# Performance work log

Measured on AMD Instinct MI355X. Metric: run time of the kernel, lower is better.

Reference implementation:

```python
import jax, jax.numpy as jnp
import numpy as np

D_MODEL = 256
NHEAD = 4
HEAD_DIM = D_MODEL // NHEAD
TEMP = float(np.sqrt(D_MODEL / NHEAD))
EPS = 1e-5


def layernorm(x, g, b):
    mu = jnp.mean(x, axis=-1, keepdims=True)
    var = jnp.mean(jnp.square(x - mu), axis=-1, keepdims=True)
    return (x - mu) * jax.lax.rsqrt(var + EPS) * g + b


def setup_inputs() -> dict:
    key = jax.random.key(0)
    ks = jax.random.split(key, 8)
    B, S, D = 4, 4096, D_MODEL
    s = 1.0 / np.sqrt(D)
    return {
        "x": jax.random.normal(ks[0], (B, S, D), dtype=jnp.float32),
        "Wq": jax.random.normal(ks[1], (D, D), dtype=jnp.float32) * s,
        "Wk": jax.random.normal(ks[2], (D, D), dtype=jnp.float32) * s,
        "Wv": jax.random.normal(ks[3], (D, D), dtype=jnp.float32) * s,
        "g1": jnp.ones((D,), jnp.float32),
        "b1": jnp.zeros((D,), jnp.float32),
        "g2": jnp.ones((D,), jnp.float32),
        "b2": jnp.zeros((D,), jnp.float32),
        "W1": jax.random.normal(ks[4], (D, D), dtype=jnp.float32) * s,
        "bf1": jnp.zeros((D,), jnp.float32),
        "W2": jax.random.normal(ks[5], (D, D), dtype=jnp.float32) * s,
        "bf2": jnp.zeros((D,), jnp.float32),
    }


def reference(x, Wq, Wk, Wv, g1, b1, g2, b2, W1, bf1, W2, bf2):
    B, S, D = x.shape
    xn = layernorm(x, g1, b1)
    # torch Linear (no bias): y = x @ W.T
    q = (xn @ Wq.T).reshape(B, S, NHEAD, HEAD_DIM)
    k = (xn @ Wk.T).reshape(B, S, NHEAD, HEAD_DIM)
    v = (xn @ Wv.T).reshape(B, S, NHEAD, HEAD_DIM)
    scores = jnp.einsum("bqhd,bkhd->bhqk", q, k) / TEMP
    causal = jnp.tril(jnp.ones((S, S), dtype=bool))  # True = keep
    scores = jnp.where(causal, scores, -jnp.inf)
    attn = jax.nn.softmax(scores, axis=-1)
    att = jnp.einsum("bhqk,bkhd->bqhd", attn, v).reshape(B, S, D)
    xt = x + att
    h = layernorm(xt, g2, b2)
    ffn = jax.nn.relu(h @ W1.T + bf1) @ W2.T + bf2
    return xt + ffn
```

## Files before the change

### kernel.cpp

```cpp
#include <hip/hip_runtime.h>
#include <math.h>

#define D_MODEL 256
#define NHEAD 4
#define HEAD_DIM 64
#define SEQ 4096
#define BATCH 4
#define MROWS (BATCH * SEQ)

typedef __attribute__((ext_vector_type(8))) short short8;
typedef __attribute__((ext_vector_type(4))) short short4v;
typedef __attribute__((ext_vector_type(8))) __bf16 bf16x8;
typedef __attribute__((ext_vector_type(4))) float f32x4;

__device__ inline short f2bf(float f) {
  unsigned u = __float_as_uint(f);
  u += 0x7fffu + ((u >> 16) & 1u);
  return (short)(u >> 16);
}
__device__ inline bf16x8 as_bf8(short8 s) {
  union { short8 s; bf16x8 b; } u;
  u.s = s;
  return u.b;
}
__device__ __forceinline__ void g2lds16(const void* g, void* l) {
  __builtin_amdgcn_global_load_lds(
      (const __attribute__((address_space(1))) unsigned int*)g,
      (__attribute__((address_space(3))) unsigned int*)l, 16, 0, 0);
}

__device__ __forceinline__ f32x4 mfma16bf(short4v a, short4v b, f32x4 c) {
#if __has_builtin(__builtin_amdgcn_mfma_f32_16x16x16bf16_1k)
  return __builtin_amdgcn_mfma_f32_16x16x16bf16_1k(a, b, c, 0, 0, 0);
#else
  asm("v_mfma_f32_16x16x16_bf16 %0, %1, %2, %0" : "+v"(c) : "v"(a), "v"(b));
  return c;
#endif
}

#define QSCALE 0.1803368801111204f

__global__ __launch_bounds__(256) void wcvt(const float* __restrict__ s0, const float* __restrict__ s1,
                                            const float* __restrict__ s2, const float* __restrict__ s3,
                                            const float* __restrict__ s4, short* __restrict__ d0,
                                            short* __restrict__ d1, short* __restrict__ d2,
                                            short* __restrict__ d3, short* __restrict__ d4) {
  int mat = blockIdx.x >> 5;
  int e = ((blockIdx.x & 31) * 256 + threadIdx.x) * 8;
  const float* s = mat == 0 ? s0 : mat == 1 ? s1 : mat == 2 ? s2 : mat == 3 ? s3 : s4;
  short* d = mat == 0 ? d0 : mat == 1 ? d1 : mat == 2 ? d2 : mat == 3 ? d3 : d4;
  int n = e >> 8, k0 = e & 255;
  float4 f0 = *(const float4*)(s + n * 256 + k0);
  float4 f1 = *(const float4*)(s + n * 256 + k0 + 4);
  short8 o = {f2bf(f0.x), f2bf(f0.y), f2bf(f0.z), f2bf(f0.w),
              f2bf(f1.x), f2bf(f1.y), f2bf(f1.z), f2bf(f1.w)};
  int chunk = k0 >> 5, g = (k0 >> 3) & 3;
  *(short8*)(d + n * 256 + chunk * 32 + ((g ^ (n & 3)) * 8)) = o;
}

__global__ __launch_bounds__(256) void ln_sw(const float* __restrict__ x,
                                             const float* __restrict__ g,
                                             const float* __restrict__ b,
                                             short* __restrict__ o) {
  int r = threadIdx.x >> 5, c8 = threadIdx.x & 31;
  int row = blockIdx.x * 8 + r;
  const float* xr = x + (size_t)row * D_MODEL + c8 * 8;
  float4 a = *(const float4*)xr;
  float4 c = *(const float4*)(xr + 4);
  float s = a.x + a.y + a.z + a.w + c.x + c.y + c.z + c.w;
#pragma unroll
  for (int off = 16; off > 0; off >>= 1) s += __shfl_xor(s, off);
  float mu = s * (1.0f / D_MODEL);
  float d0 = a.x - mu, d1 = a.y - mu, d2 = a.z - mu, d3 = a.w - mu;
  float d4 = c.x - mu, d5 = c.y - mu, d6 = c.z - mu, d7 = c.w - mu;
  float ss = d0 * d0 + d1 * d1 + d2 * d2 + d3 * d3 + d4 * d4 + d5 * d5 + d6 * d6 + d7 * d7;
#pragma unroll
  for (int off = 16; off > 0; off >>= 1) ss += __shfl_xor(ss, off);
  float rstd = rsqrtf(ss * (1.0f / D_MODEL) + 1e-5f);
  float4 ga = *(const float4*)(g + c8 * 8);
  float4 gc = *(const float4*)(g + c8 * 8 + 4);
  float4 ba = *(const float4*)(b + c8 * 8);
  float4 bc = *(const float4*)(b + c8 * 8 + 4);
  short8 ov = {f2bf(d0 * rstd * ga.x + ba.x), f2bf(d1 * rstd * ga.y + ba.y),
               f2bf(d2 * rstd * ga.z + ba.z), f2bf(d3 * rstd * ga.w + ba.w),
               f2bf(d4 * rstd * gc.x + bc.x), f2bf(d5 * rstd * gc.y + bc.y),
               f2bf(d6 * rstd * gc.z + bc.z), f2bf(d7 * rstd * gc.w + bc.w)};
  int chunk = c8 >> 2, gr = c8 & 3;
  *(short8*)(o + (size_t)row * D_MODEL + chunk * 32 + ((gr ^ (row & 3)) * 8)) = ov;
}

__global__ __launch_bounds__(256) void qkv_direct(
    const short* __restrict__ Wqi, const short* __restrict__ Wki,
    const short* __restrict__ Wvi, const short* __restrict__ Xn,
    short* __restrict__ qo, short* __restrict__ kimg, short* __restrict__ vimg) {
  __shared__ __align__(16) short Xs[64 * 256];
  const int t = threadIdx.x, lane = t & 63, w = t >> 6;
  const int l15 = lane & 15, quad = lane >> 4;
  const int m0 = blockIdx.x * 64;
  const int which = blockIdx.y;
  const short* Wb = which == 0 ? Wqi : which == 1 ? Wki : Wvi;

#pragma unroll
  for (int j = 0; j < 8; j++) {
    int so = __builtin_amdgcn_readfirstlane((w * 8 + j) * 512);
    g2lds16(Xn + (size_t)m0 * D_MODEL + so + lane * 8, &Xs[so]);
  }
  __syncthreads();

  const short* xb = &Xs[l15 * 256 + ((quad ^ (l15 & 3)) * 8)];
  const short* wb = Wb + (size_t)(w * 64 + l15) * 256 + ((quad ^ (l15 & 3)) * 8);

  f32x4 acc[4][4];
#pragma unroll
  for (int i = 0; i < 4; i++)
#pragma unroll
    for (int j = 0; j < 4; j++) acc[i][j] = (f32x4){0.f, 0.f, 0.f, 0.f};

#pragma unroll
  for (int kf = 0; kf < 8; kf++) {
    bf16x8 fx[4], fw[4];
#pragma unroll
    for (int i = 0; i < 4; i++) {
      fx[i] = as_bf8(*(const short8*)(xb + i * 4096 + kf * 32));
      fw[i] = as_bf8(*(const short8*)(wb + i * 4096 + kf * 32));
    }
    if (which == 2) {
#pragma unroll
      for (int mt = 0; mt < 4; mt++)
#pragma unroll
        for (int nt = 0; nt < 4; nt++)
          acc[mt][nt] = __builtin_amdgcn_mfma_f32_16x16x32_bf16(fx[mt], fw[nt], acc[mt][nt], 0, 0, 0);
    } else {
#pragma unroll
      for (int mt = 0; mt < 4; mt++)
#pragma unroll
        for (int nt = 0; nt < 4; nt++)
          acc[mt][nt] = __builtin_amdgcn_mfma_f32_16x16x32_bf16(fw[nt], fx[mt], acc[mt][nt], 0, 0, 0);
    }
  }

#pragma unroll
  for (int mt = 0; mt < 4; mt++)
#pragma unroll
    for (int nt = 0; nt < 4; nt++) {
      f32x4 v = acc[mt][nt];
      if (which == 2) {
        int n = w * 64 + nt * 16 + l15;
        int mr = m0 + mt * 16 + quad * 4;
        int b = mr >> 12, s = mr & 4095, h = n >> 6, d = n & 63;
        size_t off = ((size_t)(b * NHEAD + h) * 64 + (s >> 6)) * 4096 +
                     (size_t)d * 64 + ((((s & 63) >> 3) ^ (d & 7)) * 8) + (s & 7);
        short4v o = {f2bf(v[0]), f2bf(v[1]), f2bf(v[2]), f2bf(v[3])};
        *(short4v*)(vimg + off) = o;
      } else {
        int m = m0 + mt * 16 + l15;
        int nb = w * 64 + nt * 16 + quad * 4;
        if (which == 0) {
          v *= QSCALE;
          short4v o = {f2bf(v[0]), f2bf(v[1]), f2bf(v[2]), f2bf(v[3])};
          *(short4v*)(qo + (size_t)m * D_MODEL + nb) = o;
        } else {
          int b = m >> 12, s = m & 4095, h = nb >> 6, d = nb & 63;
          size_t off = ((size_t)(b * NHEAD + h) * 64 + (s >> 6)) * 4096 +
                       (size_t)(s & 63) * 64 + (((d >> 3) ^ (s & 7)) * 8) + (d & 7);
          short4v o = {f2bf(v[0]), f2bf(v[1]), f2bf(v[2]), f2bf(v[3])};
          *(short4v*)(kimg + off) = o;
        }
      }
    }
}

__global__ __launch_bounds__(256) void ffn_direct(
    const short* __restrict__ w1i, const short* __restrict__ w2i,
    const short* __restrict__ Hsw, const float* __restrict__ bf1,
    const float* __restrict__ bf2, const float* __restrict__ xt,
    float* __restrict__ out) {
  __shared__ __align__(16) short Hs[32 * 256];
  __shared__ __align__(16) short F1s[32 * 264];
  const int t = threadIdx.x, lane = t & 63, w = t >> 6;
  const int l15 = lane & 15, quad = lane >> 4;
  const int m0 = blockIdx.x * 32;

#pragma unroll
  for (int j = 0; j < 4; j++) {
    int so = __builtin_amdgcn_readfirstlane((w * 4 + j) * 512);
    g2lds16(Hsw + (size_t)m0 * D_MODEL + so + lane * 8, &Hs[so]);
  }
  __syncthreads();

  const short* hb = &Hs[l15 * 256 + ((quad ^ (l15 & 3)) * 8)];
  const short* w1b = w1i + (size_t)(w * 64 + l15) * 256 + ((quad ^ (l15 & 3)) * 8);
  const short* w2b = w2i + (size_t)(w * 64 + l15) * 256 + ((quad ^ (l15 & 3)) * 8);

  f32x4 a1[2][4];
#pragma unroll
  for (int i = 0; i < 2; i++)
#pragma unroll
    for (int j = 0; j < 4; j++) a1[i][j] = (f32x4){0.f, 0.f, 0.f, 0.f};
#pragma unroll
  for (int kf = 0; kf < 8; kf++) {
    bf16x8 fh[2], fw1[4];
#pragma unroll
    for (int i = 0; i < 2; i++) fh[i] = as_bf8(*(const short8*)(hb + i * 4096 + kf * 32));
#pragma unroll
    for (int i = 0; i < 4; i++) fw1[i] = as_bf8(*(const short8*)(w1b + i * 4096 + kf * 32));
#pragma unroll
    for (int mt = 0; mt < 2; mt++)
#pragma unroll
      for (int nt = 0; nt < 4; nt++)
        a1[mt][nt] = __builtin_amdgcn_mfma_f32_16x16x32_bf16(fw1[nt], fh[mt], a1[mt][nt], 0, 0, 0);
  }
#pragma unroll
  for (int mt = 0; mt < 2; mt++)
#pragma unroll
    for (int nt = 0; nt < 4; nt++) {
      int n1 = w * 64 + nt * 16 + quad * 4;
      int ml = mt * 16 + l15;
      float4 bv = *(const float4*)(bf1 + n1);
      f32x4 v = a1[mt][nt];
      short4v o = {f2bf(fmaxf(v[0] + bv.x, 0.f)), f2bf(fmaxf(v[1] + bv.y, 0.f)),
                   f2bf(fmaxf(v[2] + bv.z, 0.f)), f2bf(fmaxf(v[3] + bv.w, 0.f))};
      *(short4v*)&F1s[ml * 264 + n1] = o;
    }
  __syncthreads();

  const short* fb = &F1s[l15 * 264 + quad * 8];
  f32x4 a2[2][4];
#pragma unroll
  for (int i = 0; i < 2; i++)
#pragma unroll
    for (int j = 0; j < 4; j++) a2[i][j] = (f32x4){0.f, 0.f, 0.f, 0.f};
#pragma unroll
  for (int kf = 0; kf < 8; kf++) {
    bf16x8 ff[2], fw2[4];
#pragma unroll
    for (int i = 0; i < 2; i++) ff[i] = as_bf8(*(const short8*)(fb + i * 16 * 264 + kf * 32));
#pragma unroll
    for (int i = 0; i < 4; i++) fw2[i] = as_bf8(*(const short8*)(w2b + i * 4096 + kf * 32));
#pragma unroll
    for (int mt = 0; mt < 2; mt++)
#pragma unroll
      for (int nt = 0; nt < 4; nt++)
        a2[mt][nt] = __builtin_amdgcn_mfma_f32_16x16x32_bf16(ff[mt], fw2[nt], a2[mt][nt], 0, 0, 0);
  }
#pragma unroll
  for (int mt = 0; mt < 2; mt++)
#pragma unroll
    for (int nt = 0; nt < 4; nt++) {
      int n2 = w * 64 + nt * 16 + l15;
      int mg = m0 + mt * 16 + quad * 4;
      float bv = bf2[n2];
      f32x4 v = a2[mt][nt];
#pragma unroll
      for (int r = 0; r < 4; r++) {
        size_t a = (size_t)(mg + r) * D_MODEL + n2;
        out[a] = v[r] + bv + xt[a];
      }
    }
}

__global__ __launch_bounds__(256, 3) void attn_v7(const short* __restrict__ qb,
                                                  const short* __restrict__ kimg,
                                                  const short* __restrict__ vimg,
                                                  const float* __restrict__ x,
                                                  float* __restrict__ xt) {
  __shared__ __align__(16) short Ks[2 * 4096];
  __shared__ __align__(16) short Vs[2 * 4096];

  const int t = threadIdx.x, lane = t & 63, w = t >> 6;
  const int quad = lane >> 4, l15 = lane & 15, l7 = lane & 7;
  const int qa = quad & 1, q1 = quad >> 1;
  const int yy = blockIdx.y, gq = yy >> 4, rq = yy & 15;
  const int qt = gq == 0 ? 63 - rq : gq == 1 ? rq : gq == 2 ? 47 - rq : 16 + rq;
  const int bh = blockIdx.x, b = bh >> 2, h = bh & 3;
  const int ldsoff = __builtin_amdgcn_readfirstlane(w * 512);
  const short* kb_bh = kimg + (size_t)bh * 64 * 4096;
  const short* vb_bh = vimg + (size_t)bh * 64 * 4096;

  const int sb = w * 32;
  const int q0 = qt * 64;

  const short* ka[2][2];
#pragma unroll
  for (int kk = 0; kk < 2; kk++)
#pragma unroll
    for (int dh = 0; dh < 2; dh++)
      ka[kk][dh] = &Ks[(sb + kk * 16 + l15) * 64 + (((quad + 4 * dh) ^ l7) * 8)];
  const short* va[2];
#pragma unroll
  for (int kk = 0; kk < 2; kk++) {
    int sk = sb + kk * 16;
    va[kk] = &Vs[(sk >> 6) * 4096 + l15 * 64 + ((((((sk & 63) >> 3) | q1) ^ l7)) * 8) + qa * 4];
  }

  bf16x8 qf[4][2];
  {
    const short* qpb = qb + ((size_t)(b * SEQ + q0 + l15)) * D_MODEL + h * HEAD_DIM + quad * 8;
#pragma unroll
    for (int qq = 0; qq < 4; qq++) {
      qf[qq][0] = as_bf8(*(const short8*)(qpb + qq * 16 * D_MODEL));
      qf[qq][1] = as_bf8(*(const short8*)(qpb + qq * 16 * D_MODEL + 32));
    }
  }

  f32x4 oacc[4][4];
#pragma unroll
  for (int i = 0; i < 4; i++)
#pragma unroll
    for (int j = 0; j < 4; j++) oacc[i][j] = (f32x4){0.f, 0.f, 0.f, 0.f};
  float lrun[4] = {0.f, 0.f, 0.f, 0.f};

  const int niter = (qt + 2) >> 1;

#pragma unroll
  for (int i = 0; i < 4; i++) {
    g2lds16(kb_bh + i * 2048 + t * 8, &Ks[i * 2048 + ldsoff]);
    g2lds16(vb_bh + i * 2048 + t * 8, &Vs[i * 2048 + ldsoff]);
  }
  __syncthreads();

  for (int it = 0; it < niter; it++) {
    const int j0 = it * 128;
    const bool active = (j0 + sb) <= (q0 + 63);

    uint2 pu[2][4];
    if (active) {
      f32x4 st[2][4];
#pragma unroll
      for (int kk = 0; kk < 2; kk++) {
        bf16x8 k0 = as_bf8(*(const short8*)(ka[kk][0]));
        bf16x8 k1 = as_bf8(*(const short8*)(ka[kk][1]));
#pragma unroll
        for (int qq = 0; qq < 4; qq++) {
          f32x4 z = (f32x4){0.f, 0.f, 0.f, 0.f};
          z = __builtin_amdgcn_mfma_f32_16x16x32_bf16(k0, qf[qq][0], z, 0, 0, 0);
          z = __builtin_amdgcn_mfma_f32_16x16x32_bf16(k1, qf[qq][1], z, 0, 0, 0);
          st[kk][qq] = z;
        }
      }
      if (j0 + sb + 31 > q0) {
#pragma unroll
        for (int kk = 0; kk < 2; kk++) {
          int kbase = j0 + sb + kk * 16 + quad * 4;
#pragma unroll
          for (int qq = 0; qq < 4; qq++) {
            int qrow = q0 + qq * 16 + l15;
#pragma unroll
            for (int r = 0; r < 4; r++)
              if (kbase + r > qrow) st[kk][qq][r] = -1e30f;
          }
        }
      }
#pragma unroll
      for (int kk = 0; kk < 2; kk++)
#pragma unroll
        for (int qq = 0; qq < 4; qq++) {
          float p0 = __builtin_amdgcn_exp2f(st[kk][qq][0]);
          float p1 = __builtin_amdgcn_exp2f(st[kk][qq][1]);
          float p2 = __builtin_amdgcn_exp2f(st[kk][qq][2]);
          float p3 = __builtin_amdgcn_exp2f(st[kk][qq][3]);
          lrun[qq] += p0 + p1 + p2 + p3;
          pu[kk][qq].x = (__float_as_uint(p0) >> 16) | (__float_as_uint(p1) & 0xffff0000u);
          pu[kk][qq].y = (__float_as_uint(p2) >> 16) | (__float_as_uint(p3) & 0xffff0000u);
        }
    }

    __syncthreads();

    if (it + 1 < niter) {
      const short* kc_base = kb_bh + (size_t)(2 * (it + 1)) * 4096;
#pragma unroll
      for (int i = 0; i < 4; i++)
        g2lds16(kc_base + i * 2048 + t * 8, &Ks[i * 2048 + ldsoff]);
    }

    if (active) {
#pragma unroll
      for (int kk = 0; kk < 2; kk++) {
        union { uint2 u; short4v s; } pb0, pb1, pb2, pb3;
        pb0.u = pu[kk][0];
        pb1.u = pu[kk][1];
        pb2.u = pu[kk][2];
        pb3.u = pu[kk][3];
#pragma unroll
        for (int dt = 0; dt < 4; dt++) {
          short4v vv = *(const short4v*)(va[kk] + dt * 1024);
          oacc[dt][0] = mfma16bf(vv, pb0.s, oacc[dt][0]);
          oacc[dt][1] = mfma16bf(vv, pb1.s, oacc[dt][1]);
          oacc[dt][2] = mfma16bf(vv, pb2.s, oacc[dt][2]);
          oacc[dt][3] = mfma16bf(vv, pb3.s, oacc[dt][3]);
        }
      }
    }

    __syncthreads();

    if (it + 1 < niter) {
      const short* vc_base = vb_bh + (size_t)(2 * (it + 1)) * 4096;
#pragma unroll
      for (int i = 0; i < 4; i++)
        g2lds16(vc_base + i * 2048 + t * 8, &Vs[i * 2048 + ldsoff]);
    }
  }

#pragma unroll
  for (int qq = 0; qq < 4; qq++) {
    lrun[qq] += __shfl_xor(lrun[qq], 16);
    lrun[qq] += __shfl_xor(lrun[qq], 32);
  }
  float* ored = (float*)Ks;
  float* lred = (float*)Vs;
  __syncthreads();
  if (quad == 0) {
#pragma unroll
    for (int qq = 0; qq < 4; qq++) lred[(w * 4 + qq) * 16 + l15] = lrun[qq];
  }
#pragma unroll
  for (int rr = 1; rr < 4; rr++) {
#pragma unroll
    for (int dt = 0; dt < 4; dt++)
      if (dt == ((w + rr) & 3)) {
#pragma unroll
        for (int qq = 0; qq < 4; qq++)
#pragma unroll
          for (int e = 0; e < 4; e++)
            ored[dt * 1024 + (quad * 4 + e) * 64 + qq * 16 + l15] = oacc[dt][qq][e];
      }
    __syncthreads();
#pragma unroll
    for (int dt = 0; dt < 4; dt++)
      if (dt == w) {
#pragma unroll
        for (int qq = 0; qq < 4; qq++)
#pragma unroll
          for (int e = 0; e < 4; e++)
            oacc[dt][qq][e] += ored[dt * 1024 + (quad * 4 + e) * 64 + qq * 16 + l15];
      }
    if (rr < 3) __syncthreads();
  }
  float inv[4];
#pragma unroll
  for (int qq = 0; qq < 4; qq++) {
    float s = lred[qq * 16 + l15] + lred[(4 + qq) * 16 + l15] +
              lred[(8 + qq) * 16 + l15] + lred[(12 + qq) * 16 + l15];
    inv[qq] = 1.0f / s;
  }
#pragma unroll
  for (int dt = 0; dt < 4; dt++)
    if (dt == w) {
      size_t rowb = ((size_t)(b * SEQ + q0 + l15)) * D_MODEL + h * HEAD_DIM + dt * 16 + quad * 4;
#pragma unroll
      for (int qq = 0; qq < 4; qq++) {
        size_t a = rowb + (size_t)qq * 16 * D_MODEL;
        float4 xv = *(const float4*)(x + a);
        float4 o = make_float4(oacc[dt][qq][0] * inv[qq] + xv.x,
                               oacc[dt][qq][1] * inv[qq] + xv.y,
                               oacc[dt][qq][2] * inv[qq] + xv.z,
                               oacc[dt][qq][3] * inv[qq] + xv.w);
        *(float4*)(xt + a) = o;
      }
    }
}

extern "C" void kernel_launch(void* const* d_in, const int* in_sizes, int n_in,
                              void* d_out, int out_size, void* d_ws,
                              size_t ws_size, hipStream_t stream) {
  const float* x = (const float*)d_in[0];
  const float* Wq = (const float*)d_in[1];
  const float* Wk = (const float*)d_in[2];
  const float* Wv = (const float*)d_in[3];
  const float* g1 = (const float*)d_in[4];
  const float* b1 = (const float*)d_in[5];
  const float* g2 = (const float*)d_in[6];
  const float* b2 = (const float*)d_in[7];
  const float* W1 = (const float*)d_in[8];
  const float* bf1 = (const float*)d_in[9];
  const float* W2 = (const float*)d_in[10];
  const float* bf2 = (const float*)d_in[11];
  float* out = (float*)d_out;

  char* ws = (char*)d_ws;
  float* xt = (float*)ws;
  short* q_bf = (short*)(ws + (16u << 20));
  short* kimg = (short*)(ws + (24u << 20));
  short* vimg = (short*)(ws + (32u << 20));
  short* xn_sw = (short*)(ws + (40u << 20));
  short* wq_i = (short*)(ws + (48u << 20));
  short* wk_i = wq_i + 65536;
  short* wv_i = wq_i + 2 * 65536;
  short* w1_i = wq_i + 3 * 65536;
  short* w2_i = wq_i + 4 * 65536;

  dim3 blk(256);
  wcvt<<<160, blk, 0, stream>>>(Wq, Wk, Wv, W1, W2, wq_i, wk_i, wv_i, w1_i, w2_i);
  ln_sw<<<MROWS / 8, blk, 0, stream>>>(x, g1, b1, xn_sw);
  qkv_direct<<<dim3(MROWS / 64, 3), blk, 0, stream>>>(wq_i, wk_i, wv_i, xn_sw,
                                                      q_bf, kimg, vimg);
  attn_v7<<<dim3(16, 64), blk, 0, stream>>>(q_bf, kimg, vimg, x, xt);
  ln_sw<<<MROWS / 8, blk, 0, stream>>>(xt, g2, b2, xn_sw);
  ffn_direct<<<MROWS / 32, blk, 0, stream>>>(w1_i, w2_i, xn_sw, bf1, bf2, xt, out);
}
```

Baseline: 184.8 us.

## Register-prefetch K/V in attention and fuse second LayerNorm into FFN

The attention kernel no longer stages K/V tiles through shared memory with block-wide barriers. Each wave now loads its own K and V fragments straight from global memory into registers, double-buffered, so the next tile is fetched while the current one is being computed. This removes the per-iteration __syncthreads but raises register pressure, so launch bounds drop to 2 blocks per SM. Separately, the second LayerNorm is computed inside the FFN kernel, which removes one launch and the bf16 round trip of the normalized activations through global memory.

```diff
diff --git a/kernel.cpp b/kernel.cpp
--- a/kernel.cpp
+++ b/kernel.cpp
@@ -170,21 +170,46 @@
     }
 }
 
-__global__ __launch_bounds__(256) void ffn_direct(
+__global__ __launch_bounds__(256) void ffn_ln(
     const short* __restrict__ w1i, const short* __restrict__ w2i,
-    const short* __restrict__ Hsw, const float* __restrict__ bf1,
-    const float* __restrict__ bf2, const float* __restrict__ xt,
-    float* __restrict__ out) {
+    const float* __restrict__ g2v, const float* __restrict__ b2v,
+    const float* __restrict__ bf1, const float* __restrict__ bf2,
+    const float* __restrict__ xt, float* __restrict__ out) {
   __shared__ __align__(16) short Hs[32 * 256];
   __shared__ __align__(16) short F1s[32 * 264];
   const int t = threadIdx.x, lane = t & 63, w = t >> 6;
   const int l15 = lane & 15, quad = lane >> 4;
   const int m0 = blockIdx.x * 32;
 
-#pragma unroll
-  for (int j = 0; j < 4; j++) {
-    int so = __builtin_amdgcn_readfirstlane((w * 4 + j) * 512);
-    g2lds16(Hsw + (size_t)m0 * D_MODEL + so + lane * 8, &Hs[so]);
+  {
+    const int r = t >> 5, c8 = t & 31;
+    float4 ga = *(const float4*)(g2v + c8 * 8);
+    float4 gc = *(const float4*)(g2v + c8 * 8 + 4);
+    float4 ba = *(const float4*)(b2v + c8 * 8);
+    float4 bc = *(const float4*)(b2v + c8 * 8 + 4);
+#pragma unroll
+    for (int pass = 0; pass < 4; pass++) {
+      int row = pass * 8 + r;
+      const float* xr = xt + (size_t)(m0 + row) * D_MODEL + c8 * 8;
+      float4 a = *(const float4*)xr;
+      float4 c = *(const float4*)(xr + 4);
+      float s = a.x + a.y + a.z + a.w + c.x + c.y + c.z + c.w;
+#pragma unroll
+      for (int off = 16; off > 0; off >>= 1) s += __shfl_xor(s, off);
+      float mu = s * (1.0f / D_MODEL);
+      float d0 = a.x - mu, d1 = a.y - mu, d2 = a.z - mu, d3 = a.w - mu;
+      float d4 = c.x - mu, d5 = c.y - mu, d6 = c.z - mu, d7 = c.w - mu;
+      float ss = d0 * d0 + d1 * d1 + d2 * d2 + d3 * d3 + d4 * d4 + d5 * d5 + d6 * d6 + d7 * d7;
+#pragma unroll
+      for (int off = 16; off > 0; off >>= 1) ss += __shfl_xor(ss, off);
+      float rstd = rsqrtf(ss * (1.0f / D_MODEL) + 1e-5f);
+      short8 ov = {f2bf(d0 * rstd * ga.x + ba.x), f2bf(d1 * rstd * ga.y + ba.y),
+                   f2bf(d2 * rstd * ga.z + ba.z), f2bf(d3 * rstd * ga.w + ba.w),
+                   f2bf(d4 * rstd * gc.x + bc.x), f2bf(d5 * rstd * gc.y + bc.y),
+                   f2bf(d6 * rstd * gc.z + bc.z), f2bf(d7 * rstd * gc.w + bc.w)};
+      int chunk = c8 >> 2, gr = c8 & 3;
+      *(short8*)&Hs[row * 256 + chunk * 32 + ((gr ^ (row & 3)) * 8)] = ov;
+    }
   }
   __syncthreads();
 
@@ -259,13 +284,13 @@
     }
 }
 
-__global__ __launch_bounds__(256, 3) void attn_v7(const short* __restrict__ qb,
+__global__ __launch_bounds__(256, 2) void attn_v8(const short* __restrict__ qb,
                                                   const short* __restrict__ kimg,
                                                   const short* __restrict__ vimg,
                                                   const float* __restrict__ x,
                                                   float* __restrict__ xt) {
-  __shared__ __align__(16) short Ks[2 * 4096];
-  __shared__ __align__(16) short Vs[2 * 4096];
+  __shared__ __align__(16) float ored[4 * 1024];
+  __shared__ float lred[256];
 
   const int t = threadIdx.x, lane = t & 63, w = t >> 6;
   const int quad = lane >> 4, l15 = lane & 15, l7 = lane & 7;
@@ -273,24 +298,23 @@
   const int yy = blockIdx.y, gq = yy >> 4, rq = yy & 15;
   const int qt = gq == 0 ? 63 - rq : gq == 1 ? rq : gq == 2 ? 47 - rq : 16 + rq;
   const int bh = blockIdx.x, b = bh >> 2, h = bh & 3;
-  const int ldsoff = __builtin_amdgcn_readfirstlane(w * 512);
   const short* kb_bh = kimg + (size_t)bh * 64 * 4096;
   const short* vb_bh = vimg + (size_t)bh * 64 * 4096;
 
   const int sb = w * 32;
   const int q0 = qt * 64;
 
-  const short* ka[2][2];
+  int koff[2][2];
 #pragma unroll
   for (int kk = 0; kk < 2; kk++)
 #pragma unroll
     for (int dh = 0; dh < 2; dh++)
-      ka[kk][dh] = &Ks[(sb + kk * 16 + l15) * 64 + (((quad + 4 * dh) ^ l7) * 8)];
-  const short* va[2];
+      koff[kk][dh] = (sb + kk * 16 + l15) * 64 + (((quad + 4 * dh) ^ l7) * 8);
+  int voff[2];
 #pragma unroll
   for (int kk = 0; kk < 2; kk++) {
     int sk = sb + kk * 16;
-    va[kk] = &Vs[(sk >> 6) * 4096 + l15 * 64 + ((((((sk & 63) >> 3) | q1) ^ l7)) * 8) + qa * 4];
+    voff[kk] = (sk >> 6) * 4096 + l15 * 64 + ((((sk & 63) >> 3) | q1) ^ l7) * 8 + qa * 4;
   }
 
   bf16x8 qf[4][2];
@@ -312,24 +336,31 @@
 
   const int niter = (qt + 2) >> 1;
 
-#pragma unroll
-  for (int i = 0; i < 4; i++) {
-    g2lds16(kb_bh + i * 2048 + t * 8, &Ks[i * 2048 + ldsoff]);
-    g2lds16(vb_bh + i * 2048 + t * 8, &Vs[i * 2048 + ldsoff]);
-  }
-  __syncthreads();
-
-  for (int it = 0; it < niter; it++) {
+  bf16x8 kA[2][2], kB[2][2];
+  short4v vA[2][4], vB[2][4];
+
+  if (sb <= q0 + 63) {
+#pragma unroll
+    for (int kk = 0; kk < 2; kk++) {
+#pragma unroll
+      for (int dh = 0; dh < 2; dh++)
+        kA[kk][dh] = as_bf8(*(const short8*)(kb_bh + koff[kk][dh]));
+#pragma unroll
+      for (int dt = 0; dt < 4; dt++)
+        vA[kk][dt] = *(const short4v*)(vb_bh + voff[kk] + dt * 1024);
+    }
+  }
+
+  auto body = [&](bf16x8(&KC)[2][2], short4v(&VC)[2][4], bf16x8(&KN)[2][2],
+                  short4v(&VN)[2][4], int it) {
     const int j0 = it * 128;
     const bool active = (j0 + sb) <= (q0 + 63);
-
-    uint2 pu[2][4];
+    const bool pnext = (it + 1 < niter) && ((j0 + 128 + sb) <= (q0 + 63));
+    f32x4 st[2][4];
     if (active) {
-      f32x4 st[2][4];
 #pragma unroll
       for (int kk = 0; kk < 2; kk++) {
-        bf16x8 k0 = as_bf8(*(const short8*)(ka[kk][0]));
-        bf16x8 k1 = as_bf8(*(const short8*)(ka[kk][1]));
+        bf16x8 k0 = KC[kk][0], k1 = KC[kk][1];
 #pragma unroll
         for (int qq = 0; qq < 4; qq++) {
           f32x4 z = (f32x4){0.f, 0.f, 0.f, 0.f};
@@ -338,6 +369,21 @@
           st[kk][qq] = z;
         }
       }
+    }
+    if (pnext) {
+      const short* kbp = kb_bh + (size_t)(it + 1) * 8192;
+      const short* vbp = vb_bh + (size_t)(it + 1) * 8192;
+#pragma unroll
+      for (int kk = 0; kk < 2; kk++) {
+#pragma unroll
+        for (int dh = 0; dh < 2; dh++)
+          KN[kk][dh] = as_bf8(*(const short8*)(kbp + koff[kk][dh]));
+#pragma unroll
+        for (int dt = 0; dt < 4; dt++)
+          VN[kk][dt] = *(const short4v*)(vbp + voff[kk] + dt * 1024);
+      }
+    }
+    if (active) {
       if (j0 + sb + 31 > q0) {
 #pragma unroll
         for (int kk = 0; kk < 2; kk++) {
@@ -351,6 +397,7 @@
           }
         }
       }
+      uint2 pu[2][4];
 #pragma unroll
       for (int kk = 0; kk < 2; kk++)
 #pragma unroll
@@ -363,18 +410,6 @@
           pu[kk][qq].x = (__float_as_uint(p0) >> 16) | (__float_as_uint(p1) & 0xffff0000u);
           pu[kk][qq].y = (__float_as_uint(p2) >> 16) | (__float_as_uint(p3) & 0xffff0000u);
         }
-    }
-
-    __syncthreads();
-
-    if (it + 1 < niter) {
-      const short* kc_base = kb_bh + (size_t)(2 * (it + 1)) * 4096;
-#pragma unroll
-      for (int i = 0; i < 4; i++)
-        g2lds16(kc_base + i * 2048 + t * 8, &Ks[i * 2048 + ldsoff]);
-    }
-
-    if (active) {
 #pragma unroll
       for (int kk = 0; kk < 2; kk++) {
         union { uint2 u; short4v s; } pb0, pb1, pb2, pb3;
@@ -384,7 +419,7 @@
         pb3.u = pu[kk][3];
 #pragma unroll
         for (int dt = 0; dt < 4; dt++) {
-          short4v vv = *(const short4v*)(va[kk] + dt * 1024);
+          short4v vv = VC[kk][dt];
           oacc[dt][0] = mfma16bf(vv, pb0.s, oacc[dt][0]);
           oacc[dt][1] = mfma16bf(vv, pb1.s, oacc[dt][1]);
           oacc[dt][2] = mfma16bf(vv, pb2.s, oacc[dt][2]);
@@ -392,15 +427,14 @@
         }
       }
     }
-
-    __syncthreads();
-
-    if (it + 1 < niter) {
-      const short* vc_base = vb_bh + (size_t)(2 * (it + 1)) * 4096;
-#pragma unroll
-      for (int i = 0; i < 4; i++)
-        g2lds16(vc_base + i * 2048 + t * 8, &Vs[i * 2048 + ldsoff]);
-    }
+  };
+
+  int it = 0;
+  while (true) {
+    body(kA, vA, kB, vB, it);
+    if (++it >= niter) break;
+    body(kB, vB, kA, vA, it);
+    if (++it >= niter) break;
   }
 
 #pragma unroll
@@ -408,9 +442,6 @@
     lrun[qq] += __shfl_xor(lrun[qq], 16);
     lrun[qq] += __shfl_xor(lrun[qq], 32);
   }
-  float* ored = (float*)Ks;
-  float* lred = (float*)Vs;
-  __syncthreads();
   if (quad == 0) {
 #pragma unroll
     for (int qq = 0; qq < 4; qq++) lred[(w * 4 + qq) * 16 + l15] = lrun[qq];
@@ -496,7 +527,6 @@
   ln_sw<<<MROWS / 8, blk, 0, stream>>>(x, g1, b1, xn_sw);
   qkv_direct<<<dim3(MROWS / 64, 3), blk, 0, stream>>>(wq_i, wk_i, wv_i, xn_sw,
                                                       q_bf, kimg, vimg);
-  attn_v7<<<dim3(16, 64), blk, 0, stream>>>(q_bf, kimg, vimg, x, xt);
-  ln_sw<<<MROWS / 8, blk, 0, stream>>>(xt, g2, b2, xn_sw);
-  ffn_direct<<<MROWS / 32, blk, 0, stream>>>(w1_i, w2_i, xn_sw, bf1, bf2, xt, out);
-}
+  attn_v8<<<dim3(16, 64), blk, 0, stream>>>(q_bf, kimg, vimg, x, xt);
+  ffn_ln<<<MROWS / 32, blk, 0, stream>>>(w1_i, w2_i, g2, b2, bf1, bf2, xt, out);
+}
```

Measured after the change: 176.7 us. 1.05x faster.
